# Kernel tuning notes

Hardware: AMD Instinct MI355X
Metric: run time of the kernel (lower is better)

## Reference

```python
import jax, jax.numpy as jnp
import numpy as np

B, S, D, F, E = 8, 4096, 512, 2048, 8
INIT_LAMBDA = 0.2
LN_EPS = 1e-5
LN_MERGE = 0.03  # scale used when merging layer_norm expert task-vectors


def setup_inputs() -> dict:
    key = jax.random.key(0)
    ks = jax.random.split(key, 12)
    n = lambda k, shp, s=1.0: jax.random.normal(k, shp, dtype=jnp.float32) * s
    return {
        "hidden_states": n(ks[0], (B, S, D)),
        # DictMoEGate (2 hidden layers): fc1 ~ N(0, 0.01), fc2 bias = init_lambda
        "gfc1_w": n(ks[1], (D, D), 0.01),
        "gfc1_b": jnp.zeros((D,), jnp.float32),
        "gfc2_w": n(ks[2], (E, D), 0.01),
        "gfc2_b": jnp.full((E,), INIT_LAMBDA, dtype=jnp.float32),
        # base PositionWiseFeedForward params (torch Linear layout: [out, in])
        "W1": n(ks[3], (F, D), 0.02),
        "b1": jnp.zeros((F,), jnp.float32),
        "W2": n(ks[4], (D, F), 0.02),
        "b2": jnp.zeros((D,), jnp.float32),
        "ln_g": jnp.ones((D,), jnp.float32),
        "ln_b": jnp.zeros((D,), jnp.float32),
        # expert task vectors (expert_sd - base_sd), one per base param
        "tv_W1": n(ks[5], (E, F, D), 0.02),
        "tv_b1": n(ks[6], (E, F), 0.02),
        "tv_W2": n(ks[7], (E, D, F), 0.02),
        "tv_b2": n(ks[8], (E, D), 0.02),
        "tv_ln_g": n(ks[9], (E, D), 0.02),
        "tv_ln_b": n(ks[10], (E, D), 0.02),
    }


def reference(hidden_states, gfc1_w, gfc1_b, gfc2_w, gfc2_b,
              W1, b1, W2, b2, ln_g, ln_b,
              tv_W1, tv_b1, tv_W2, tv_b2, tv_ln_g, tv_ln_b):
    x = hidden_states  # [B, S, D] (batch_first)
    # --- gate: per-token 2-layer MLP, then mean over sequence -> [B, E] ---
    gh = jax.nn.relu(jnp.einsum('bsd,hd->bsh', x, gfc1_w) + gfc1_b)
    g = (jnp.einsum('bsh,eh->bse', gh, gfc2_w) + gfc2_b).mean(axis=1)  # [B, E]
    # --- per-sample merged weights: base + sum_e g[b,e] * task_vector[e] ---
    W1m = W1 + jnp.einsum('be,efd->bfd', g, tv_W1)   # [B, F, D]
    b1m = b1 + g @ tv_b1                              # [B, F]
    W2m = W2 + jnp.einsum('be,edf->bdf', g, tv_W2)   # [B, D, F]
    b2m = b2 + g @ tv_b2                              # [B, D]
    # layer_norm params: sd = param + sum_e (tv_e - param) * 0.03 (gate-independent)
    lng = ln_g + LN_MERGE * (tv_ln_g - ln_g).sum(axis=0)  # [D]
    lnb = ln_b + LN_MERGE * (tv_ln_b - ln_b).sum(axis=0)  # [D]
    # --- PositionWiseFeedForward with per-sample weights (dropout = eval/identity) ---
    h = jax.nn.relu(jnp.einsum('bsd,bfd->bsf', x, W1m) + b1m[:, None, :])  # [B, S, F]
    out = jnp.einsum('bsf,bdf->bsd', h, W2m) + b2m[:, None, :]             # [B, S, D]
    res = x + out
    mu = res.mean(axis=-1, keepdims=True)
    var = res.var(axis=-1, keepdims=True)
    return (res - mu) * jax.lax.rsqrt(var + LN_EPS) * lng + lnb
```

## Files before the change

### kernel.cpp

```cpp
#include <hip/hip_runtime.h>

typedef __bf16 bf16;
typedef __attribute__((ext_vector_type(4))) __bf16 bf16x4;
typedef __attribute__((ext_vector_type(8))) __bf16 bf16x8;
typedef __attribute__((ext_vector_type(4))) float f32x4;

#define LDS16(gp, lp)                                                          \
  __builtin_amdgcn_global_load_lds(                                            \
      (const __attribute__((address_space(1))) void*)(gp),                     \
      (__attribute__((address_space(3))) void*)(lp), 16, 0, 0)

__global__ __launch_bounds__(256) void prep_kernel(const float* __restrict__ x,
                                                   const float* __restrict__ g1w,
                                                   bf16* __restrict__ x_bf,
                                                   bf16* __restrict__ g1w_bf,
                                                   float* __restrict__ ghsum) {
  const int bid = blockIdx.x;
  if (bid < 8320) {
    const float* src = bid < 8192 ? x : g1w;
    bf16* dst = bid < 8192 ? x_bf : g1w_bf;
    const int base = bid < 8192 ? bid : bid - 8192;
    int i = (base * 256 + threadIdx.x) * 8;
    float4 a = *(const float4*)(src + i);
    float4 b = *(const float4*)(src + i + 4);
    bf16x8 v;
    v[0] = (bf16)a.x; v[1] = (bf16)a.y; v[2] = (bf16)a.z; v[3] = (bf16)a.w;
    v[4] = (bf16)b.x; v[5] = (bf16)b.y; v[6] = (bf16)b.z; v[7] = (bf16)b.w;
    *(bf16x8*)(dst + i) = v;
  } else {
    float4 z = make_float4(0.f, 0.f, 0.f, 0.f);
    float* p = ghsum + threadIdx.x * 16;
#pragma unroll
    for (int k = 0; k < 4; ++k) *(float4*)(p + k * 4) = z;
  }
}

template <int MODE, int NT>
__global__ __launch_bounds__(512) void gemm256(const bf16* __restrict__ A,
                                               const bf16* __restrict__ B0, long bstride,
                                               const float* __restrict__ bias, long biasStride,
                                               const float* __restrict__ resid,
                                               float* __restrict__ fout,
                                               bf16* __restrict__ hout) {
  constexpr int K = NT * 32;
  __shared__ __align__(16) bf16 smem[2 * 16384];
  const int tid = threadIdx.x;
  const int lane = tid & 63, wv = tid >> 6;
  const int wm = wv >> 2, wn = wv & 3;
  const int lr = lane & 15, q = lane >> 4;
  const int b = blockIdx.z;
  const long blockM = (long)b * 4096 + (long)blockIdx.x * 256;
  const int blockN = blockIdx.y * 256;
  const bf16* Ab = A + blockM * K;
  const bf16* Bb = B0 + (long)b * bstride + (long)blockN * K;

  const int s4 = lane >> 2;
  const int cch = ((lane & 3) ^ ((s4 >> 1) & 3)) * 8;
  const int gA0 = wv * 2;
  const int qa = q ^ ((lr >> 1) & 3);
  const int aoff = (wm * 128 + lr) * 32 + qa * 8;
  const int boff = (wn * 64 + lr) * 32 + qa * 8;

  f32x4 acc[8][4] = {};

  auto stage = [&](int t) {
    bf16* As = smem + (t & 1) * 16384;
    bf16* Bs = As + 8192;
    const long k0 = (long)t * 32;
#pragma unroll
    for (int li = 0; li < 2; ++li) {
      const int g = gA0 + li;
      LDS16(Ab + (long)(g * 16 + s4) * K + k0 + cch, As + g * 512);
      LDS16(Bb + (long)(g * 16 + s4) * K + k0 + cch, Bs + g * 512);
    }
  };

  stage(0);
  __syncthreads();

#pragma unroll 1
  for (int t = 0; t < NT; ++t) {
    if (t + 1 < NT) stage(t + 1);
    const bf16* As = smem + (t & 1) * 16384;
    const bf16* Bs = As + 8192;
    bf16x8 af[8], bfr[4];
#pragma unroll
    for (int j = 0; j < 4; ++j) bfr[j] = *(const bf16x8*)&Bs[boff + j * 512];
#pragma unroll
    for (int i = 0; i < 8; ++i) af[i] = *(const bf16x8*)&As[aoff + i * 512];
#pragma unroll
    for (int i = 0; i < 8; ++i)
#pragma unroll
      for (int j = 0; j < 4; ++j)
        acc[i][j] = __builtin_amdgcn_mfma_f32_16x16x32_bf16(af[i], bfr[j], acc[i][j], 0, 0, 0);
    __syncthreads();
  }

  if (MODE == 0) {
#pragma unroll
    for (int j = 0; j < 4; ++j) {
      const int gc = blockN + wn * 64 + j * 16 + lr;
      const float bv = bias[gc];
      float s = 0.f;
#pragma unroll
      for (int i = 0; i < 8; ++i)
#pragma unroll
        for (int r = 0; r < 4; ++r) {
          float v = acc[i][j][r] + bv;
          s += v > 0.f ? v : 0.f;
        }
      s += __shfl_xor(s, 16);
      s += __shfl_xor(s, 32);
      if (q == 0) atomicAdd(&fout[b * 512 + gc], s);
    }
  } else if (MODE == 1) {
    float bvv[4];
#pragma unroll
    for (int j = 0; j < 4; ++j)
      bvv[j] = bias[(long)b * biasStride + blockN + wn * 64 + j * 16 + lr];
#pragma unroll 1
    for (int half = 0; half < 2; ++half) {
      __syncthreads();
      if (wm == half) {
#pragma unroll
        for (int i = 0; i < 8; ++i)
#pragma unroll
          for (int j = 0; j < 4; ++j)
#pragma unroll
            for (int r = 0; r < 4; ++r) {
              const int row = i * 16 + q * 4 + r;
              const int col = wn * 64 + j * 16 + lr;
              float v = acc[i][j][r] + bvv[j];
              smem[row * 256 + col] = (bf16)(v > 0.f ? v : 0.f);
            }
      }
      __syncthreads();
#pragma unroll
      for (int p = 0; p < 8; ++p) {
        const int row = p * 16 + (tid >> 5);
        const int seg = tid & 31;
        *(bf16x8*)&hout[(blockM + half * 128 + row) * 2048 + blockN + seg * 8] =
            *(const bf16x8*)&smem[row * 256 + seg * 8];
      }
    }
  } else {
#pragma unroll
    for (int j = 0; j < 4; ++j) {
      const int gc = blockN + wn * 64 + j * 16 + lr;
      const float bv = bias[(long)b * biasStride + gc];
#pragma unroll
      for (int i = 0; i < 8; ++i)
#pragma unroll
        for (int r = 0; r < 4; ++r) {
          const long gr = blockM + wm * 128 + i * 16 + q * 4 + r;
          fout[gr * 512 + gc] = acc[i][j][r] + bv + resid[gr * 512 + gc];
        }
    }
  }
}

__global__ __launch_bounds__(512) void small_kernel(
    const float* __restrict__ ghsum, const float* __restrict__ g2w,
    const float* __restrict__ g2b, const float* __restrict__ lngI,
    const float* __restrict__ lnbI, const float* __restrict__ tvlg,
    const float* __restrict__ tvlb, const float* __restrict__ b1,
    const float* __restrict__ tvb1, const float* __restrict__ b2,
    const float* __restrict__ tvb2, float* __restrict__ g, float* __restrict__ lng,
    float* __restrict__ lnb, float* __restrict__ b1m, float* __restrict__ b2m) {
  __shared__ float gs[64];
  const int t = threadIdx.x;
  if (t < 64) {
    const int b = t >> 3, e = t & 7;
    float s = 0.f;
    for (int h = 0; h < 512; ++h) s += ghsum[b * 512 + h] * g2w[e * 512 + h];
    float gv = s * (1.f / 4096.f) + g2b[e];
    gs[t] = gv;
    g[t] = gv;
  }
  __syncthreads();
  if (t < 512) {
    float lg = lngI[t], lb = lnbI[t], sg = 0.f, sb = 0.f;
    for (int e = 0; e < 8; ++e) { sg += tvlg[e * 512 + t]; sb += tvlb[e * 512 + t]; }
    lng[t] = lg + 0.03f * (sg - 8.f * lg);
    lnb[t] = lb + 0.03f * (sb - 8.f * lb);
  }
  for (int i = t; i < 8 * 2048; i += 512) {
    const int b = i >> 11, f = i & 2047;
    float s = b1[f];
    for (int e = 0; e < 8; ++e) s += gs[b * 8 + e] * tvb1[e * 2048 + f];
    b1m[i] = s;
  }
  for (int i = t; i < 8 * 512; i += 512) {
    const int b = i >> 9, d = i & 511;
    float s = b2[d];
    for (int e = 0; e < 8; ++e) s += gs[b * 8 + e] * tvb2[e * 512 + d];
    b2m[i] = s;
  }
}

__global__ __launch_bounds__(256) void merge_kernel(
    const float* __restrict__ W1, const float* __restrict__ tvW1,
    const float* __restrict__ W2, const float* __restrict__ tvW2,
    const float* __restrict__ g, bf16* __restrict__ W1m, bf16* __restrict__ W2m) {
  int idx = (blockIdx.x * 256 + threadIdx.x) * 4;
  const float* Wp;
  const float* tvp;
  bf16* outp;
  if (idx < 1048576) {
    Wp = W1; tvp = tvW1; outp = W1m;
  } else {
    idx -= 1048576;
    Wp = W2; tvp = tvW2; outp = W2m;
  }
  float4 w = *(const float4*)(Wp + idx);
  float4 tv[8];
#pragma unroll
  for (int e = 0; e < 8; ++e) tv[e] = *(const float4*)(tvp + (long)e * 1048576 + idx);
#pragma unroll
  for (int b = 0; b < 8; ++b) {
    float4 s = w;
#pragma unroll
    for (int e = 0; e < 8; ++e) {
      const float ge = g[b * 8 + e];
      s.x += ge * tv[e].x; s.y += ge * tv[e].y;
      s.z += ge * tv[e].z; s.w += ge * tv[e].w;
    }
    bf16x4 o;
    o[0] = (bf16)s.x; o[1] = (bf16)s.y; o[2] = (bf16)s.z; o[3] = (bf16)s.w;
    *(bf16x4*)(outp + (long)b * 1048576 + idx) = o;
  }
}

__global__ __launch_bounds__(256) void ln_kernel(float* __restrict__ out,
                                                 const float* __restrict__ lng,
                                                 const float* __restrict__ lnb) {
  const int wv = threadIdx.x >> 6, lane = threadIdx.x & 63;
  const long row = (long)blockIdx.x * 4 + wv;
  float* p = out + row * 512 + lane * 8;
  float4 a = *(float4*)p;
  float4 b = *(float4*)(p + 4);
  float v[8] = {a.x, a.y, a.z, a.w, b.x, b.y, b.z, b.w};
  float s1 = 0.f, s2 = 0.f;
#pragma unroll
  for (int k = 0; k < 8; ++k) { s1 += v[k]; s2 += v[k] * v[k]; }
#pragma unroll
  for (int off = 32; off > 0; off >>= 1) {
    s1 += __shfl_xor(s1, off);
    s2 += __shfl_xor(s2, off);
  }
  const float mean = s1 * (1.f / 512.f);
  const float var = s2 * (1.f / 512.f) - mean * mean;
  const float rstd = rsqrtf(var + 1e-5f);
  const int c = lane * 8;
  float o[8];
#pragma unroll
  for (int k = 0; k < 8; ++k) o[k] = (v[k] - mean) * rstd * lng[c + k] + lnb[c + k];
  *(float4*)p = make_float4(o[0], o[1], o[2], o[3]);
  *(float4*)(p + 4) = make_float4(o[4], o[5], o[6], o[7]);
}

extern "C" void kernel_launch(void* const* d_in, const int* in_sizes, int n_in,
                              void* d_out, int out_size, void* d_ws, size_t ws_size,
                              hipStream_t stream) {
  const float* x    = (const float*)d_in[0];
  const float* g1w  = (const float*)d_in[1];
  const float* g1b  = (const float*)d_in[2];
  const float* g2w  = (const float*)d_in[3];
  const float* g2b  = (const float*)d_in[4];
  const float* W1   = (const float*)d_in[5];
  const float* b1   = (const float*)d_in[6];
  const float* W2   = (const float*)d_in[7];
  const float* b2   = (const float*)d_in[8];
  const float* lngI = (const float*)d_in[9];
  const float* lnbI = (const float*)d_in[10];
  const float* tvW1 = (const float*)d_in[11];
  const float* tvb1 = (const float*)d_in[12];
  const float* tvW2 = (const float*)d_in[13];
  const float* tvb2 = (const float*)d_in[14];
  const float* tvlg = (const float*)d_in[15];
  const float* tvlb = (const float*)d_in[16];
  float* out = (float*)d_out;

  char* w = (char*)d_ws;
  bf16*  x_bf   = (bf16*)(w);
  bf16*  g1w_bf = (bf16*)(w + 33554432);
  bf16*  W1m    = (bf16*)(w + 34078720);
  bf16*  W2m    = (bf16*)(w + 50855936);
  bf16*  h      = (bf16*)(w + 67633152);
  float* ghsum  = (float*)(w + 201850880);
  float* g      = (float*)(w + 201867264);
  float* b1m    = (float*)(w + 201867520);
  float* b2m    = (float*)(w + 201933056);
  float* lng    = (float*)(w + 201949440);
  float* lnb    = (float*)(w + 201951488);

  prep_kernel<<<8321, 256, 0, stream>>>(x, g1w, x_bf, g1w_bf, ghsum);
  gemm256<0, 16><<<dim3(16, 2, 8), 512, 0, stream>>>(x_bf, g1w_bf, 0, g1b, 0,
                                                     nullptr, ghsum, nullptr);
  small_kernel<<<1, 512, 0, stream>>>(ghsum, g2w, g2b, lngI, lnbI, tvlg, tvlb,
                                      b1, tvb1, b2, tvb2, g, lng, lnb, b1m, b2m);
  merge_kernel<<<2048, 256, 0, stream>>>(W1, tvW1, W2, tvW2, g, W1m, W2m);
  gemm256<1, 16><<<dim3(16, 8, 8), 512, 0, stream>>>(x_bf, W1m, 1048576, b1m, 2048,
                                                     nullptr, nullptr, h);
  gemm256<2, 64><<<dim3(16, 2, 8), 512, 0, stream>>>(h, W2m, 1048576, b2m, 512,
                                                     x, out, nullptr);
  ln_kernel<<<8192, 256, 0, stream>>>(out, lng, lnb);
}
```

Baseline: 456.3 us.

## Shrink GEMM tiles to 128x128 with 256 threads and batch-interleaved 1D grid

Replaces the 256x256-tile, 512-thread GEMM with a 128x128-tile, 256-thread variant that uses half the LDS and accumulators and asks for 3 blocks per CU. The grid becomes 1D with batch index in the low bits, so concurrently running blocks span all batches. The goal is more blocks in flight to fill the CUs, since the old grid had only 256 blocks for the gate and down GEMMs. The MODE 1 epilogue is simplified to a single LDS staging pass. In exchange, each tile does less reuse, so operand traffic per FLOP from global memory and LDS goes up.

```diff
diff --git a/kernel.cpp b/kernel.cpp
--- a/kernel.cpp
+++ b/kernel.cpp
@@ -36,21 +36,25 @@
 }
 
 template <int MODE, int NT>
-__global__ __launch_bounds__(512) void gemm256(const bf16* __restrict__ A,
-                                               const bf16* __restrict__ B0, long bstride,
-                                               const float* __restrict__ bias, long biasStride,
-                                               const float* __restrict__ resid,
-                                               float* __restrict__ fout,
-                                               bf16* __restrict__ hout) {
+__global__ __launch_bounds__(256, 3) void gemm128(const bf16* __restrict__ A,
+                                                  const bf16* __restrict__ B0, long bstride,
+                                                  const float* __restrict__ bias, long biasStride,
+                                                  const float* __restrict__ resid,
+                                                  float* __restrict__ fout,
+                                                  bf16* __restrict__ hout) {
   constexpr int K = NT * 32;
-  __shared__ __align__(16) bf16 smem[2 * 16384];
+  __shared__ __align__(16) bf16 smem[2 * 8192];
   const int tid = threadIdx.x;
   const int lane = tid & 63, wv = tid >> 6;
-  const int wm = wv >> 2, wn = wv & 3;
+  const int wm = wv >> 1, wn = wv & 1;
   const int lr = lane & 15, q = lane >> 4;
-  const int b = blockIdx.z;
-  const long blockM = (long)b * 4096 + (long)blockIdx.x * 256;
-  const int blockN = blockIdx.y * 256;
+  const int bid = blockIdx.x;
+  const int b = bid & 7;
+  const int r = bid >> 3;
+  const int mb = r & 31;
+  const int nb = r >> 5;
+  const long blockM = (long)b * 4096 + (long)mb * 128;
+  const int blockN = nb * 128;
   const bf16* Ab = A + blockM * K;
   const bf16* Bb = B0 + (long)b * bstride + (long)blockN * K;
 
@@ -58,14 +62,14 @@
   const int cch = ((lane & 3) ^ ((s4 >> 1) & 3)) * 8;
   const int gA0 = wv * 2;
   const int qa = q ^ ((lr >> 1) & 3);
-  const int aoff = (wm * 128 + lr) * 32 + qa * 8;
+  const int aoff = (wm * 64 + lr) * 32 + qa * 8;
   const int boff = (wn * 64 + lr) * 32 + qa * 8;
 
-  f32x4 acc[8][4] = {};
+  f32x4 acc[4][4] = {};
 
   auto stage = [&](int t) {
-    bf16* As = smem + (t & 1) * 16384;
-    bf16* Bs = As + 8192;
+    bf16* As = smem + (t & 1) * 8192;
+    bf16* Bs = As + 4096;
     const long k0 = (long)t * 32;
 #pragma unroll
     for (int li = 0; li < 2; ++li) {
@@ -81,15 +85,15 @@
 #pragma unroll 1
   for (int t = 0; t < NT; ++t) {
     if (t + 1 < NT) stage(t + 1);
-    const bf16* As = smem + (t & 1) * 16384;
-    const bf16* Bs = As + 8192;
-    bf16x8 af[8], bfr[4];
+    const bf16* As = smem + (t & 1) * 8192;
+    const bf16* Bs = As + 4096;
+    bf16x8 af[4], bfr[4];
 #pragma unroll
     for (int j = 0; j < 4; ++j) bfr[j] = *(const bf16x8*)&Bs[boff + j * 512];
 #pragma unroll
-    for (int i = 0; i < 8; ++i) af[i] = *(const bf16x8*)&As[aoff + i * 512];
-#pragma unroll
-    for (int i = 0; i < 8; ++i)
+    for (int i = 0; i < 4; ++i) af[i] = *(const bf16x8*)&As[aoff + i * 512];
+#pragma unroll
+    for (int i = 0; i < 4; ++i)
 #pragma unroll
       for (int j = 0; j < 4; ++j)
         acc[i][j] = __builtin_amdgcn_mfma_f32_16x16x32_bf16(af[i], bfr[j], acc[i][j], 0, 0, 0);
@@ -103,10 +107,10 @@
       const float bv = bias[gc];
       float s = 0.f;
 #pragma unroll
-      for (int i = 0; i < 8; ++i)
-#pragma unroll
-        for (int r = 0; r < 4; ++r) {
-          float v = acc[i][j][r] + bv;
+      for (int i = 0; i < 4; ++i)
+#pragma unroll
+        for (int r2 = 0; r2 < 4; ++r2) {
+          float v = acc[i][j][r2] + bv;
           s += v > 0.f ? v : 0.f;
         }
       s += __shfl_xor(s, 16);
@@ -114,34 +118,26 @@
       if (q == 0) atomicAdd(&fout[b * 512 + gc], s);
     }
   } else if (MODE == 1) {
-    float bvv[4];
-#pragma unroll
-    for (int j = 0; j < 4; ++j)
-      bvv[j] = bias[(long)b * biasStride + blockN + wn * 64 + j * 16 + lr];
-#pragma unroll 1
-    for (int half = 0; half < 2; ++half) {
-      __syncthreads();
-      if (wm == half) {
-#pragma unroll
-        for (int i = 0; i < 8; ++i)
-#pragma unroll
-          for (int j = 0; j < 4; ++j)
-#pragma unroll
-            for (int r = 0; r < 4; ++r) {
-              const int row = i * 16 + q * 4 + r;
-              const int col = wn * 64 + j * 16 + lr;
-              float v = acc[i][j][r] + bvv[j];
-              smem[row * 256 + col] = (bf16)(v > 0.f ? v : 0.f);
-            }
-      }
-      __syncthreads();
-#pragma unroll
-      for (int p = 0; p < 8; ++p) {
-        const int row = p * 16 + (tid >> 5);
-        const int seg = tid & 31;
-        *(bf16x8*)&hout[(blockM + half * 128 + row) * 2048 + blockN + seg * 8] =
-            *(const bf16x8*)&smem[row * 256 + seg * 8];
-      }
+#pragma unroll
+    for (int j = 0; j < 4; ++j) {
+      const int gc = wn * 64 + j * 16 + lr;
+      const float bv = bias[(long)b * biasStride + blockN + gc];
+#pragma unroll
+      for (int i = 0; i < 4; ++i)
+#pragma unroll
+        for (int r2 = 0; r2 < 4; ++r2) {
+          const int lrow = wm * 64 + i * 16 + q * 4 + r2;
+          float v = acc[i][j][r2] + bv;
+          smem[lrow * 128 + gc] = (bf16)(v > 0.f ? v : 0.f);
+        }
+    }
+    __syncthreads();
+#pragma unroll
+    for (int p = 0; p < 8; ++p) {
+      const int row = p * 16 + (tid >> 4);
+      const int col = (tid & 15) * 8;
+      *(bf16x8*)&hout[(blockM + row) * 2048 + blockN + col] =
+          *(const bf16x8*)&smem[row * 128 + col];
     }
   } else {
 #pragma unroll
@@ -149,11 +145,11 @@
       const int gc = blockN + wn * 64 + j * 16 + lr;
       const float bv = bias[(long)b * biasStride + gc];
 #pragma unroll
-      for (int i = 0; i < 8; ++i)
-#pragma unroll
-        for (int r = 0; r < 4; ++r) {
-          const long gr = blockM + wm * 128 + i * 16 + q * 4 + r;
-          fout[gr * 512 + gc] = acc[i][j][r] + bv + resid[gr * 512 + gc];
+      for (int i = 0; i < 4; ++i)
+#pragma unroll
+        for (int r2 = 0; r2 < 4; ++r2) {
+          const long gr = blockM + wm * 64 + i * 16 + q * 4 + r2;
+          fout[gr * 512 + gc] = acc[i][j][r2] + bv + resid[gr * 512 + gc];
         }
     }
   }
@@ -295,14 +291,14 @@
   float* lnb    = (float*)(w + 201951488);
 
   prep_kernel<<<8321, 256, 0, stream>>>(x, g1w, x_bf, g1w_bf, ghsum);
-  gemm256<0, 16><<<dim3(16, 2, 8), 512, 0, stream>>>(x_bf, g1w_bf, 0, g1b, 0,
-                                                     nullptr, ghsum, nullptr);
+  gemm128<0, 16><<<1024, 256, 0, stream>>>(x_bf, g1w_bf, 0, g1b, 0,
+                                           nullptr, ghsum, nullptr);
   small_kernel<<<1, 512, 0, stream>>>(ghsum, g2w, g2b, lngI, lnbI, tvlg, tvlb,
                                       b1, tvb1, b2, tvb2, g, lng, lnb, b1m, b2m);
   merge_kernel<<<2048, 256, 0, stream>>>(W1, tvW1, W2, tvW2, g, W1m, W2m);
-  gemm256<1, 16><<<dim3(16, 8, 8), 512, 0, stream>>>(x_bf, W1m, 1048576, b1m, 2048,
-                                                     nullptr, nullptr, h);
-  gemm256<2, 64><<<dim3(16, 2, 8), 512, 0, stream>>>(h, W2m, 1048576, b2m, 512,
-                                                     x, out, nullptr);
+  gemm128<1, 16><<<4096, 256, 0, stream>>>(x_bf, W1m, 1048576, b1m, 2048,
+                                           nullptr, nullptr, h);
+  gemm128<2, 64><<<1024, 256, 0, stream>>>(h, W2m, 1048576, b2m, 512,
+                                           x, out, nullptr);
   ln_kernel<<<8192, 256, 0, stream>>>(out, lng, lnb);
 }
```

New measurement: 514.2 us. 12.7% more time.

## Double the GEMM K-tile per stage and linearize grid with batch-interleaved block mapping

Applied to the files above, without the earlier changes.

Each main-loop iteration of the GEMM now loads and consumes a 64-wide K slice (two 32-wide sub-stages) instead of 32, halving the number of barriers and loop iterations. LDS use doubles to 128 KB per block. The 3D grid is replaced with a 1D grid whose block index is decoded with the batch as the fastest-varying dimension, so consecutive blocks land on different batches, which changes L2/MALL locality and how work spreads across XCDs. The larger LDS footprint limits occupancy to one block per CU.

```diff
diff --git a/kernel.cpp b/kernel.cpp
--- a/kernel.cpp
+++ b/kernel.cpp
@@ -42,15 +42,19 @@
                                                const float* __restrict__ resid,
                                                float* __restrict__ fout,
                                                bf16* __restrict__ hout) {
-  constexpr int K = NT * 32;
-  __shared__ __align__(16) bf16 smem[2 * 16384];
+  constexpr int K = NT * 64;
+  __shared__ __align__(16) bf16 smem[2 * 32768];
   const int tid = threadIdx.x;
   const int lane = tid & 63, wv = tid >> 6;
   const int wm = wv >> 2, wn = wv & 3;
   const int lr = lane & 15, q = lane >> 4;
-  const int b = blockIdx.z;
-  const long blockM = (long)b * 4096 + (long)blockIdx.x * 256;
-  const int blockN = blockIdx.y * 256;
+  const int bid = blockIdx.x;
+  const int b = bid & 7;
+  const int r = bid >> 3;
+  const int mb = r & 15;
+  const int nb = r >> 4;
+  const long blockM = (long)b * 4096 + (long)mb * 256;
+  const int blockN = nb * 256;
   const bf16* Ab = A + blockM * K;
   const bf16* Bb = B0 + (long)b * bstride + (long)blockN * K;
 
@@ -64,14 +68,19 @@
   f32x4 acc[8][4] = {};
 
   auto stage = [&](int t) {
-    bf16* As = smem + (t & 1) * 16384;
-    bf16* Bs = As + 8192;
-    const long k0 = (long)t * 32;
-#pragma unroll
-    for (int li = 0; li < 2; ++li) {
-      const int g = gA0 + li;
-      LDS16(Ab + (long)(g * 16 + s4) * K + k0 + cch, As + g * 512);
-      LDS16(Bb + (long)(g * 16 + s4) * K + k0 + cch, Bs + g * 512);
+    bf16* buf = smem + (t & 1) * 32768;
+    const long k0 = (long)t * 64;
+#pragma unroll
+    for (int s = 0; s < 2; ++s) {
+      bf16* As = buf + s * 16384;
+      bf16* Bs = As + 8192;
+      const long kk = k0 + s * 32;
+#pragma unroll
+      for (int li = 0; li < 2; ++li) {
+        const int g = gA0 + li;
+        LDS16(Ab + (long)(g * 16 + s4) * K + kk + cch, As + g * 512);
+        LDS16(Bb + (long)(g * 16 + s4) * K + kk + cch, Bs + g * 512);
+      }
     }
   };
 
@@ -81,18 +90,22 @@
 #pragma unroll 1
   for (int t = 0; t < NT; ++t) {
     if (t + 1 < NT) stage(t + 1);
-    const bf16* As = smem + (t & 1) * 16384;
-    const bf16* Bs = As + 8192;
-    bf16x8 af[8], bfr[4];
-#pragma unroll
-    for (int j = 0; j < 4; ++j) bfr[j] = *(const bf16x8*)&Bs[boff + j * 512];
-#pragma unroll
-    for (int i = 0; i < 8; ++i) af[i] = *(const bf16x8*)&As[aoff + i * 512];
-#pragma unroll
-    for (int i = 0; i < 8; ++i)
-#pragma unroll
-      for (int j = 0; j < 4; ++j)
-        acc[i][j] = __builtin_amdgcn_mfma_f32_16x16x32_bf16(af[i], bfr[j], acc[i][j], 0, 0, 0);
+    const bf16* buf = smem + (t & 1) * 32768;
+#pragma unroll
+    for (int s = 0; s < 2; ++s) {
+      const bf16* As = buf + s * 16384;
+      const bf16* Bs = As + 8192;
+      bf16x8 af[8], bfr[4];
+#pragma unroll
+      for (int j = 0; j < 4; ++j) bfr[j] = *(const bf16x8*)&Bs[boff + j * 512];
+#pragma unroll
+      for (int i = 0; i < 8; ++i) af[i] = *(const bf16x8*)&As[aoff + i * 512];
+#pragma unroll
+      for (int i = 0; i < 8; ++i)
+#pragma unroll
+        for (int j = 0; j < 4; ++j)
+          acc[i][j] = __builtin_amdgcn_mfma_f32_16x16x32_bf16(af[i], bfr[j], acc[i][j], 0, 0, 0);
+    }
     __syncthreads();
   }
 
@@ -105,8 +118,8 @@
 #pragma unroll
       for (int i = 0; i < 8; ++i)
 #pragma unroll
-        for (int r = 0; r < 4; ++r) {
-          float v = acc[i][j][r] + bv;
+        for (int r2 = 0; r2 < 4; ++r2) {
+          float v = acc[i][j][r2] + bv;
           s += v > 0.f ? v : 0.f;
         }
       s += __shfl_xor(s, 16);
@@ -127,10 +140,10 @@
 #pragma unroll
           for (int j = 0; j < 4; ++j)
 #pragma unroll
-            for (int r = 0; r < 4; ++r) {
-              const int row = i * 16 + q * 4 + r;
+            for (int r2 = 0; r2 < 4; ++r2) {
+              const int row = i * 16 + q * 4 + r2;
               const int col = wn * 64 + j * 16 + lr;
-              float v = acc[i][j][r] + bvv[j];
+              float v = acc[i][j][r2] + bvv[j];
               smem[row * 256 + col] = (bf16)(v > 0.f ? v : 0.f);
             }
       }
@@ -151,9 +164,9 @@
 #pragma unroll
       for (int i = 0; i < 8; ++i)
 #pragma unroll
-        for (int r = 0; r < 4; ++r) {
-          const long gr = blockM + wm * 128 + i * 16 + q * 4 + r;
-          fout[gr * 512 + gc] = acc[i][j][r] + bv + resid[gr * 512 + gc];
+        for (int r2 = 0; r2 < 4; ++r2) {
+          const long gr = blockM + wm * 128 + i * 16 + q * 4 + r2;
+          fout[gr * 512 + gc] = acc[i][j][r2] + bv + resid[gr * 512 + gc];
         }
     }
   }
@@ -295,14 +308,14 @@
   float* lnb    = (float*)(w + 201951488);
 
   prep_kernel<<<8321, 256, 0, stream>>>(x, g1w, x_bf, g1w_bf, ghsum);
-  gemm256<0, 16><<<dim3(16, 2, 8), 512, 0, stream>>>(x_bf, g1w_bf, 0, g1b, 0,
-                                                     nullptr, ghsum, nullptr);
+  gemm256<0, 8><<<256, 512, 0, stream>>>(x_bf, g1w_bf, 0, g1b, 0,
+                                         nullptr, ghsum, nullptr);
   small_kernel<<<1, 512, 0, stream>>>(ghsum, g2w, g2b, lngI, lnbI, tvlg, tvlb,
                                       b1, tvb1, b2, tvb2, g, lng, lnb, b1m, b2m);
   merge_kernel<<<2048, 256, 0, stream>>>(W1, tvW1, W2, tvW2, g, W1m, W2m);
-  gemm256<1, 16><<<dim3(16, 8, 8), 512, 0, stream>>>(x_bf, W1m, 1048576, b1m, 2048,
-                                                     nullptr, nullptr, h);
-  gemm256<2, 64><<<dim3(16, 2, 8), 512, 0, stream>>>(h, W2m, 1048576, b2m, 512,
-                                                     x, out, nullptr);
+  gemm256<1, 8><<<1024, 512, 0, stream>>>(x_bf, W1m, 1048576, b1m, 2048,
+                                          nullptr, nullptr, h);
+  gemm256<2, 32><<<256, 512, 0, stream>>>(h, W2m, 1048576, b2m, 512,
+                                          x, out, nullptr);
   ln_kernel<<<8192, 256, 0, stream>>>(out, lng, lnb);
 }
```

Result: no change. 452.5 us (-0.8%).
